# Kernel tuning notes

Hardware: AMD Instinct MI355X
Metric: run time of the kernel (lower is better)

## Reference

```python
import jax, jax.numpy as jnp
import numpy as np

B, H, L, D, BLK = 2, 16, 2048, 64, 32
NB = L // BLK          # 64 blocks per side
WINDOW = 8             # causal local window, in blocks


def make_layout():
    # [H, NB, NB] int32: block (i, j) active iff 0 <= i - j < WINDOW (causal local band)
    bi = jnp.arange(NB)
    band = ((bi[:, None] - bi[None, :]) >= 0) & ((bi[:, None] - bi[None, :]) < WINDOW)
    return jnp.broadcast_to(band[None].astype(jnp.int32), (H, NB, NB))


def setup_inputs() -> dict:
    rng = jax.random.key(0)
    kq, kk, kv, kp = jax.random.split(rng, 4)
    return {
        "query": jax.random.normal(kq, (B, H, L, D), dtype=jnp.float32),
        "key": jax.random.normal(kk, (B, H, L, D), dtype=jnp.float32),
        "value": jax.random.normal(kv, (B, H, L, D), dtype=jnp.float32),
        "key_padding_mask": jax.random.normal(kp, (B, L), dtype=jnp.float32),
        "layout": make_layout(),
    }


def reference(query, key, value, key_padding_mask, layout):
    # query/key/value: [B, H, L, D]; layout: [H, NB, NB] block sparsity pattern
    bsz, num_heads, tgt_len, head_dim = query.shape
    blk = tgt_len // layout.shape[1]
    scaling = float(head_dim) ** (-0.5)

    # SDD: scores only on active blocks. Reference computes dense then masks
    # inactive blocks to -inf, matching blocksparse softmax semantics exactly.
    scores = jnp.einsum("bhqd,bhkd->bhqk", query, key) * scaling
    # key_padding_mask_mode='add': added to logits, broadcast over queries
    scores = scores + key_padding_mask[:, None, None, :]

    # expand block layout [H, NB, NB] -> element mask [H, L, L]
    block_mask = jnp.repeat(jnp.repeat(layout.astype(bool), blk, axis=1), blk, axis=2)
    scores = jnp.where(block_mask[None], scores, -jnp.inf)

    probs = jax.nn.softmax(scores, axis=-1)  # zeros outside active blocks
    # DSD: probs @ value
    attn_output = jnp.einsum("bhqk,bhkd->bhqd", probs, value)
    return attn_output
```

## Files before the change

kernel.cpp:

```cpp
#include <hip/hip_runtime.h>

#define B_   2
#define H_   16
#define L_   2048
#define D_   64
#define BLK_ 32
#define NB_  64

#define KSW 64
#define VS  40
#define PS  40

typedef __bf16 bf16x8 __attribute__((ext_vector_type(8)));
typedef float  f32x4  __attribute__((ext_vector_type(4)));
typedef unsigned short u16x8 __attribute__((ext_vector_type(8)));

__device__ inline unsigned short f2bf(float f) {
    unsigned int u = __builtin_bit_cast(unsigned int, f);
    unsigned int r = u + 0x7fffu + ((u >> 16) & 1u);
    return (unsigned short)(r >> 16);
}

#define WG_BARRIER() asm volatile("s_waitcnt lgkmcnt(0)\n\ts_barrier" ::: "memory")

struct Tile {
    float4 k0, k1;
    float  v[8];
    float  kp0, kp1;
};

__global__ __launch_bounds__(256, 4)
void sparse_attn_kernel(const float* __restrict__ qg,
                        const float* __restrict__ kg,
                        const float* __restrict__ vg,
                        const float* __restrict__ kpm,
                        const int*   __restrict__ layout,
                        float* __restrict__ outg)
{
    __shared__ __align__(16) unsigned short Ks_[2][BLK_ * KSW];
    __shared__ __align__(16) unsigned short Vt_[2][D_ * VS];
    __shared__ __align__(16) unsigned short Ps_[4][16 * PS];

    const int tid  = threadIdx.x;
    const int wave = tid >> 6;
    const int lane = tid & 63;
    const int quad = lane >> 4;
    const int l15  = lane & 15;

    const int phys = blockIdx.x;
    const int lw   = (phys & 7) * 128 + (phys >> 3);
    const int ip = lw & 31;
    const int h  = (lw >> 5) & 15;
    const int b  = lw >> 9;
    const int i0 = ip * 2, i1 = i0 + 1;
    const int iq = i0 + (wave >> 1);

    const size_t bh = (size_t)(b * H_ + h);
    const float* kbase  = kg  + bh * L_ * D_;
    const float* vbase  = vg  + bh * L_ * D_;
    const float* kpb    = kpm + (size_t)b * L_;
    const int*   layrow = layout + (h * NB_ + iq) * NB_;

    const int jbeg = i0 - 7;

    int act[9];
    #pragma unroll
    for (int s = 0; s < 9; ++s) {
        const int j = jbeg + s;
        act[s] = (j >= 0) ? layrow[j] : 0;
    }

    bf16x8 aq[2];
    {
        const int gq = iq * BLK_ + (wave & 1) * 16 + l15;
        const float* qrow = qg + (bh * L_ + gq) * D_;
        #pragma unroll
        for (int ks = 0; ks < 2; ++ks) {
            float4 x = *(const float4*)&qrow[ks * 32 + quad * 8];
            float4 y = *(const float4*)&qrow[ks * 32 + quad * 8 + 4];
            u16x8 pk;
            pk[0]=f2bf(x.x); pk[1]=f2bf(x.y); pk[2]=f2bf(x.z); pk[3]=f2bf(x.w);
            pk[4]=f2bf(y.x); pk[5]=f2bf(y.y); pk[6]=f2bf(y.z); pk[7]=f2bf(y.w);
            aq[ks] = __builtin_bit_cast(bf16x8, pk);
        }
    }

    auto clampj = [&](int j) { return j < 0 ? 0 : j; };

    auto loadT = [&](int jc, Tile& T) {
        const float4* kb = (const float4*)(kbase + (size_t)jc * BLK_ * D_);
        T.k0 = kb[tid * 2];
        T.k1 = kb[tid * 2 + 1];
        const float* vb = vbase + (size_t)jc * BLK_ * D_;
        #pragma unroll
        for (int i = 0; i < 8; ++i) T.v[i] = vb[(wave * 8 + i) * D_ + lane];
        T.kp0 = kpb[jc * BLK_ + l15];
        T.kp1 = kpb[jc * BLK_ + 16 + l15];
    };

    auto storeT = [&](int buf, const Tile& T) {
        const int row = tid >> 3, oct = tid & 7;
        u16x8 pk;
        pk[0]=f2bf(T.k0.x); pk[1]=f2bf(T.k0.y); pk[2]=f2bf(T.k0.z); pk[3]=f2bf(T.k0.w);
        pk[4]=f2bf(T.k1.x); pk[5]=f2bf(T.k1.y); pk[6]=f2bf(T.k1.z); pk[7]=f2bf(T.k1.w);
        *(u16x8*)&Ks_[buf][row * KSW + ((oct ^ (row & 7)) * 8)] = pk;
        u16x8 pv;
        #pragma unroll
        for (int i = 0; i < 8; ++i) pv[i] = f2bf(T.v[i]);
        *(u16x8*)&Vt_[buf][lane * VS + ((wave ^ (lane & 3)) * 8)] = pv;
    };

    float lrow[4] = {0.f, 0.f, 0.f, 0.f};
    f32x4 Ot[4];
    #pragma unroll
    for (int t = 0; t < 4; ++t) Ot[t] = (f32x4){0.f, 0.f, 0.f, 0.f};

    auto computeT = [&](int buf, float kp0c, float kp1c) {
        f32x4 s0 = {0.f,0.f,0.f,0.f}, s1 = {0.f,0.f,0.f,0.f};
        #pragma unroll
        for (int ks = 0; ks < 2; ++ks) {
            const int so = ((ks * 4 + quad) ^ (l15 & 7)) * 8;
            bf16x8 b0 = *(const bf16x8*)&Ks_[buf][l15 * KSW + so];
            bf16x8 b1 = *(const bf16x8*)&Ks_[buf][(16 + l15) * KSW + so];
            s0 = __builtin_amdgcn_mfma_f32_16x16x32_bf16(aq[ks], b0, s0, 0, 0, 0);
            s1 = __builtin_amdgcn_mfma_f32_16x16x32_bf16(aq[ks], b1, s1, 0, 0, 0);
        }
        unsigned short* psw = &Ps_[wave][0];
        #pragma unroll
        for (int r = 0; r < 4; ++r) {
            float p0 = __expf(s0[r] * 0.125f + kp0c);
            float p1 = __expf(s1[r] * 0.125f + kp1c);
            lrow[r] += p0 + p1;
            const int prow = quad * 4 + r;
            psw[prow * PS + l15]      = f2bf(p0);
            psw[prow * PS + 16 + l15] = f2bf(p1);
        }
        asm volatile("s_waitcnt lgkmcnt(0)" ::: "memory");
        bf16x8 ap = *(const bf16x8*)&psw[l15 * PS + quad * 8];
        #pragma unroll
        for (int t = 0; t < 4; ++t) {
            bf16x8 bv = *(const bf16x8*)&Vt_[buf][(t * 16 + l15) * VS + ((quad ^ (l15 & 3)) * 8)];
            Ot[t] = __builtin_amdgcn_mfma_f32_16x16x32_bf16(ap, bv, Ot[t], 0, 0, 0);
        }
    };

    Tile tiles[2];
    loadT(clampj(jbeg), tiles[0]);
    storeT(0, tiles[0]);
    float kp0c = tiles[0].kp0, kp1c = tiles[0].kp1;
    loadT(clampj(jbeg + 1), tiles[1]);
    WG_BARRIER();

    int cur = 0;
    #pragma unroll
    for (int s = 0; s < 9; ++s) {
        const int j = jbeg + s;
        if (s <= 6) loadT(clampj(j + 2), tiles[s & 1]);
        if (act[s] != 0) computeT(cur, kp0c, kp1c);
        if (s < 8) {
            const Tile& T = tiles[(s + 1) & 1];
            storeT(cur ^ 1, T);
            kp0c = T.kp0; kp1c = T.kp1;
        }
        WG_BARRIER();
        cur ^= 1;
    }

    #pragma unroll
    for (int r = 0; r < 4; ++r) {
        #pragma unroll
        for (int m = 1; m < 16; m <<= 1) lrow[r] += __shfl_xor(lrow[r], m);
    }
    float* ob = outg + (bh * L_ + (size_t)iq * BLK_ + (wave & 1) * 16) * D_;
    #pragma unroll
    for (int r = 0; r < 4; ++r) {
        float inv = 1.0f / lrow[r];
        int prow = quad * 4 + r;
        #pragma unroll
        for (int t = 0; t < 4; ++t)
            ob[prow * D_ + t * 16 + l15] = Ot[t][r] * inv;
    }
}

extern "C" void kernel_launch(void* const* d_in, const int* in_sizes, int n_in,
                              void* d_out, int out_size, void* d_ws, size_t ws_size,
                              hipStream_t stream) {
    const float* q      = (const float*)d_in[0];
    const float* k      = (const float*)d_in[1];
    const float* v      = (const float*)d_in[2];
    const float* kpmask = (const float*)d_in[3];
    const int*   layout = (const int*)d_in[4];
    float* out = (float*)d_out;

    dim3 grid(B_ * H_ * (NB_ / 2));
    dim3 block(256);
    sparse_attn_kernel<<<grid, block, 0, stream>>>(q, k, v, kpmask, layout, out);
}
```

Measured before the change: 102.8 us.

## Process four query blocks per workgroup to share K/V tile loads

Each 512-thread workgroup now covers four consecutive query blocks instead of two and streams an 11-block K/V window shared by all eight waves, so the number of K/V loads and conversions per query block drops. The per-thread load and store work is halved to fit the larger block. Softmax now uses exp2 with log2e folded into the scale and the padding mask, and a native bf16 cast replaces the manual rounding routine. The trade-off is half as many workgroups, fewer resident waves per CU at 512 threads, and more barriers per workgroup.

```diff
diff --git a/kernel.cpp b/kernel.cpp
--- a/kernel.cpp
+++ b/kernel.cpp
@@ -7,29 +7,30 @@
 #define BLK_ 32
 #define NB_  64
 
+#define WGQ  4
+#define WIN  11
+#define NWG  (B_ * H_ * (NB_ / WGQ))
+
 #define KSW 64
 #define VS  40
 #define PS  40
 
 typedef __bf16 bf16x8 __attribute__((ext_vector_type(8)));
+typedef __bf16 bf16x4 __attribute__((ext_vector_type(4)));
 typedef float  f32x4  __attribute__((ext_vector_type(4)));
-typedef unsigned short u16x8 __attribute__((ext_vector_type(8)));
 
-__device__ inline unsigned short f2bf(float f) {
-    unsigned int u = __builtin_bit_cast(unsigned int, f);
-    unsigned int r = u + 0x7fffu + ((u >> 16) & 1u);
-    return (unsigned short)(r >> 16);
-}
+#define LOG2E   1.44269504088896340736f
+#define SC_LOG2 0.18033688011112042592f
 
 #define WG_BARRIER() asm volatile("s_waitcnt lgkmcnt(0)\n\ts_barrier" ::: "memory")
 
 struct Tile {
-    float4 k0, k1;
-    float  v[8];
+    float4 k0;
+    float  v[4];
     float  kp0, kp1;
 };
 
-__global__ __launch_bounds__(256, 4)
+__global__ __launch_bounds__(512, 4)
 void sparse_attn_kernel(const float* __restrict__ qg,
                         const float* __restrict__ kg,
                         const float* __restrict__ vg,
@@ -37,9 +38,9 @@
                         const int*   __restrict__ layout,
                         float* __restrict__ outg)
 {
-    __shared__ __align__(16) unsigned short Ks_[2][BLK_ * KSW];
-    __shared__ __align__(16) unsigned short Vt_[2][D_ * VS];
-    __shared__ __align__(16) unsigned short Ps_[4][16 * PS];
+    __shared__ __align__(16) __bf16 Ks_[2][BLK_ * KSW];
+    __shared__ __align__(16) __bf16 Vt_[2][D_ * VS];
+    __shared__ __align__(16) __bf16 Ps_[8][16 * PS];
 
     const int tid  = threadIdx.x;
     const int wave = tid >> 6;
@@ -48,11 +49,11 @@
     const int l15  = lane & 15;
 
     const int phys = blockIdx.x;
-    const int lw   = (phys & 7) * 128 + (phys >> 3);
-    const int ip = lw & 31;
-    const int h  = (lw >> 5) & 15;
-    const int b  = lw >> 9;
-    const int i0 = ip * 2, i1 = i0 + 1;
+    const int lw   = (phys & 7) * 64 + (phys >> 3);
+    const int ip = lw & 15;
+    const int h  = (lw >> 4) & 15;
+    const int b  = lw >> 8;
+    const int i0 = ip * WGQ;
     const int iq = i0 + (wave >> 1);
 
     const size_t bh = (size_t)(b * H_ + h);
@@ -63,11 +64,11 @@
 
     const int jbeg = i0 - 7;
 
-    int act[9];
+    unsigned int actmask = 0;
     #pragma unroll
-    for (int s = 0; s < 9; ++s) {
+    for (int s = 0; s < WIN; ++s) {
         const int j = jbeg + s;
-        act[s] = (j >= 0) ? layrow[j] : 0;
+        if (j >= 0 && layrow[j]) actmask |= (1u << s);
     }
 
     bf16x8 aq[2];
@@ -78,10 +79,10 @@
         for (int ks = 0; ks < 2; ++ks) {
             float4 x = *(const float4*)&qrow[ks * 32 + quad * 8];
             float4 y = *(const float4*)&qrow[ks * 32 + quad * 8 + 4];
-            u16x8 pk;
-            pk[0]=f2bf(x.x); pk[1]=f2bf(x.y); pk[2]=f2bf(x.z); pk[3]=f2bf(x.w);
-            pk[4]=f2bf(y.x); pk[5]=f2bf(y.y); pk[6]=f2bf(y.z); pk[7]=f2bf(y.w);
-            aq[ks] = __builtin_bit_cast(bf16x8, pk);
+            bf16x8 pk;
+            pk[0]=(__bf16)x.x; pk[1]=(__bf16)x.y; pk[2]=(__bf16)x.z; pk[3]=(__bf16)x.w;
+            pk[4]=(__bf16)y.x; pk[5]=(__bf16)y.y; pk[6]=(__bf16)y.z; pk[7]=(__bf16)y.w;
+            aq[ks] = pk;
         }
     }
 
@@ -89,25 +90,25 @@
 
     auto loadT = [&](int jc, Tile& T) {
         const float4* kb = (const float4*)(kbase + (size_t)jc * BLK_ * D_);
-        T.k0 = kb[tid * 2];
-        T.k1 = kb[tid * 2 + 1];
+        T.k0 = kb[tid];
         const float* vb = vbase + (size_t)jc * BLK_ * D_;
         #pragma unroll
-        for (int i = 0; i < 8; ++i) T.v[i] = vb[(wave * 8 + i) * D_ + lane];
-        T.kp0 = kpb[jc * BLK_ + l15];
-        T.kp1 = kpb[jc * BLK_ + 16 + l15];
+        for (int i = 0; i < 4; ++i) T.v[i] = vb[(wave * 4 + i) * D_ + lane];
+        T.kp0 = kpb[jc * BLK_ + l15]      * LOG2E;
+        T.kp1 = kpb[jc * BLK_ + 16 + l15] * LOG2E;
     };
 
     auto storeT = [&](int buf, const Tile& T) {
-        const int row = tid >> 3, oct = tid & 7;
-        u16x8 pk;
-        pk[0]=f2bf(T.k0.x); pk[1]=f2bf(T.k0.y); pk[2]=f2bf(T.k0.z); pk[3]=f2bf(T.k0.w);
-        pk[4]=f2bf(T.k1.x); pk[5]=f2bf(T.k1.y); pk[6]=f2bf(T.k1.z); pk[7]=f2bf(T.k1.w);
-        *(u16x8*)&Ks_[buf][row * KSW + ((oct ^ (row & 7)) * 8)] = pk;
-        u16x8 pv;
+        const int row = tid >> 4, f4 = tid & 15;
+        const int oct = f4 >> 1, khalf = f4 & 1;
+        bf16x4 pk;
+        pk[0]=(__bf16)T.k0.x; pk[1]=(__bf16)T.k0.y; pk[2]=(__bf16)T.k0.z; pk[3]=(__bf16)T.k0.w;
+        *(bf16x4*)&Ks_[buf][row * KSW + ((oct ^ (row & 7)) * 8) + khalf * 4] = pk;
+        bf16x4 pv;
         #pragma unroll
-        for (int i = 0; i < 8; ++i) pv[i] = f2bf(T.v[i]);
-        *(u16x8*)&Vt_[buf][lane * VS + ((wave ^ (lane & 3)) * 8)] = pv;
+        for (int i = 0; i < 4; ++i) pv[i] = (__bf16)T.v[i];
+        const int g = wave >> 1, vhalf = wave & 1;
+        *(bf16x4*)&Vt_[buf][lane * VS + ((g ^ (lane & 3)) * 8) + vhalf * 4] = pv;
     };
 
     float lrow[4] = {0.f, 0.f, 0.f, 0.f};
@@ -125,15 +126,15 @@
             s0 = __builtin_amdgcn_mfma_f32_16x16x32_bf16(aq[ks], b0, s0, 0, 0, 0);
             s1 = __builtin_amdgcn_mfma_f32_16x16x32_bf16(aq[ks], b1, s1, 0, 0, 0);
         }
-        unsigned short* psw = &Ps_[wave][0];
+        __bf16* psw = &Ps_[wave][0];
         #pragma unroll
         for (int r = 0; r < 4; ++r) {
-            float p0 = __expf(s0[r] * 0.125f + kp0c);
-            float p1 = __expf(s1[r] * 0.125f + kp1c);
+            float p0 = exp2f(fmaf(s0[r], SC_LOG2, kp0c));
+            float p1 = exp2f(fmaf(s1[r], SC_LOG2, kp1c));
             lrow[r] += p0 + p1;
             const int prow = quad * 4 + r;
-            psw[prow * PS + l15]      = f2bf(p0);
-            psw[prow * PS + 16 + l15] = f2bf(p1);
+            psw[prow * PS + l15]      = (__bf16)p0;
+            psw[prow * PS + 16 + l15] = (__bf16)p1;
         }
         asm volatile("s_waitcnt lgkmcnt(0)" ::: "memory");
         bf16x8 ap = *(const bf16x8*)&psw[l15 * PS + quad * 8];
@@ -153,11 +154,11 @@
 
     int cur = 0;
     #pragma unroll
-    for (int s = 0; s < 9; ++s) {
+    for (int s = 0; s < WIN; ++s) {
         const int j = jbeg + s;
-        if (s <= 6) loadT(clampj(j + 2), tiles[s & 1]);
-        if (act[s] != 0) computeT(cur, kp0c, kp1c);
-        if (s < 8) {
+        if (s <= WIN - 3) loadT(clampj(j + 2), tiles[s & 1]);
+        if (actmask & (1u << s)) computeT(cur, kp0c, kp1c);
+        if (s < WIN - 1) {
             const Tile& T = tiles[(s + 1) & 1];
             storeT(cur ^ 1, T);
             kp0c = T.kp0; kp1c = T.kp1;
@@ -192,7 +193,7 @@
     const int*   layout = (const int*)d_in[4];
     float* out = (float*)d_out;
 
-    dim3 grid(B_ * H_ * (NB_ / 2));
-    dim3 block(256);
+    dim3 grid(NWG);
+    dim3 block(512);
     sparse_attn_kernel<<<grid, block, 0, stream>>>(q, k, v, kpmask, layout, out);
 }
```

Result: no change. 104.0 us (+1.1%).
